# Kernel optimization log

Hardware: AMD Instinct MI355X
Metric: run time of the kernel (lower is better)

The kernel has to match this reference:

```python
import jax, jax.numpy as jnp
import numpy as np

B, S, D, H = 4, 1024, 2048, 16
DH = D // H  # 128
THETA = 10000.0


def setup_inputs() -> dict:
    key = jax.random.key(0)
    k1, k2, k3 = jax.random.split(key, 3)
    std_qkv = np.sqrt(2.0 / (D + 3 * D)).astype(np.float32)
    std_out = np.sqrt(2.0 / (D + D)).astype(np.float32)
    x = jax.random.normal(k1, (B, S, D), jnp.float32)
    w_qkv = jax.random.normal(k2, (D, 3 * D), jnp.float32) * std_qkv
    w_out = jax.random.normal(k3, (D, D), jnp.float32) * std_out
    # matrix-based RoPE table: [max_seq, d_head//2, 2, 2]
    freqs = jnp.arange(S, dtype=jnp.float32)[:, None] / THETA ** (
        2.0 * jnp.arange(DH // 2, dtype=jnp.float32) / DH)[None, :]
    eye = jnp.array([[1.0, 0.0], [0.0, 1.0]], jnp.float32)
    rot = jnp.array([[0.0, -1.0], [1.0, 0.0]], jnp.float32)
    rope_matrix = (jnp.cos(freqs)[:, :, None, None] * eye
                   + jnp.sin(freqs)[:, :, None, None] * rot)
    token_positions = jnp.arange(S, dtype=jnp.int32)
    return {"x": x, "w_qkv": w_qkv, "w_out": w_out,
            "rope_matrix": rope_matrix, "token_positions": token_positions}


def _apply_rope(t, pe):
    # t: [B, H, S, DH]; pe: [S, DH//2, 2, 2] (gathered by token_positions)
    tr = t.reshape(*t.shape[:-1], DH // 2, 2)  # interleaved (even, odd) pairs
    out = jnp.einsum('bhski,skoi->bhsko', tr, pe)
    return out.reshape(t.shape)


def reference(x, w_qkv, w_out, rope_matrix, token_positions):
    qkv = jnp.einsum('bsd,df->bsf', x, w_qkv)          # [B,S,3D]
    q, k, v = jnp.split(qkv, 3, axis=-1)
    to_heads = lambda t: t.reshape(B, S, H, DH).transpose(0, 2, 1, 3)
    q, k, v = to_heads(q), to_heads(k), to_heads(v)    # [B,H,S,DH]
    pe = rope_matrix[token_positions]                  # [S, DH//2, 2, 2]
    q = _apply_rope(q, pe)
    k = _apply_rope(k, pe)
    scores = jnp.einsum('bhqd,bhkd->bhqk', q, k) / np.float32(np.sqrt(DH))
    causal = jnp.tril(jnp.ones((S, S), dtype=bool))
    scores = jnp.where(causal, scores, -jnp.inf)
    attn = jax.nn.softmax(scores, axis=-1)
    ctx = jnp.einsum('bhqk,bhkd->bhqd', attn, v)       # [B,H,S,DH]
    ctx = ctx.transpose(0, 2, 1, 3).reshape(B, S, D)
    return jnp.einsum('bsd,df->bsf', ctx, w_out)
```

## Files before the change

### kernel.cpp

```cpp
#include <hip/hip_runtime.h>
#include <hip/hip_bf16.h>
#include <math.h>

#define Bn 4
#define Sn 1024
#define Dn 2048
#define Hn 16
#define DHn 128
#define BS (Bn * Sn)
#define QKVC (3 * Dn)

typedef __attribute__((ext_vector_type(8))) short short8;
typedef __attribute__((ext_vector_type(4))) float float4v;

__device__ inline unsigned short f2bf(float x) {
  union { float f; unsigned int u; } v; v.f = x;
  unsigned int r = v.u + 0x7fffu + ((v.u >> 16) & 1u);
  return (unsigned short)(r >> 16);
}
__device__ inline float bf2f(unsigned short b) {
  union { unsigned int u; float f; } v; v.u = ((unsigned int)b) << 16;
  return v.f;
}

__device__ __forceinline__ void gload16(const unsigned short* g, unsigned short* l) {
  __builtin_amdgcn_global_load_lds(
      (const __attribute__((address_space(1))) unsigned int*)g,
      (__attribute__((address_space(3))) unsigned int*)l, 16, 0, 0);
}

__global__ __launch_bounds__(256) void cvt_f32_bf16(
    const float* __restrict__ in, unsigned short* __restrict__ out, int n8) {
  int id = blockIdx.x * 256 + threadIdx.x;
  if (id >= n8) return;
  const float4* p = reinterpret_cast<const float4*>(in) + 2 * (size_t)id;
  float4 a = p[0], b = p[1];
  short8 o;
  o[0] = (short)f2bf(a.x); o[1] = (short)f2bf(a.y);
  o[2] = (short)f2bf(a.z); o[3] = (short)f2bf(a.w);
  o[4] = (short)f2bf(b.x); o[5] = (short)f2bf(b.y);
  o[6] = (short)f2bf(b.z); o[7] = (short)f2bf(b.w);
  *reinterpret_cast<short8*>(out + 8 * (size_t)id) = o;
}

__global__ __launch_bounds__(256) void transpose_cvt(
    const float* __restrict__ w, unsigned short* __restrict__ wT, int K, int N) {
  __shared__ unsigned short t[64][72];
  const int c0 = blockIdx.x * 64;
  const int r0 = blockIdx.y * 64;
  const int tid = threadIdx.x;
  const int r = tid >> 2;
  const int cb = (tid & 3) * 16;
#pragma unroll
  for (int it = 0; it < 4; ++it) {
    float4 v = *reinterpret_cast<const float4*>(&w[(long)(r0 + r) * N + c0 + cb + 4 * it]);
    t[r][cb + 4 * it + 0] = f2bf(v.x);
    t[r][cb + 4 * it + 1] = f2bf(v.y);
    t[r][cb + 4 * it + 2] = f2bf(v.z);
    t[r][cb + 4 * it + 3] = f2bf(v.w);
  }
  __syncthreads();
  unsigned short o[16];
#pragma unroll
  for (int e = 0; e < 16; ++e) o[e] = t[cb + e][r];
  unsigned short* dst = &wT[(long)(c0 + r) * K + r0 + cb];
  *reinterpret_cast<short8*>(dst) = *reinterpret_cast<short8*>(&o[0]);
  *reinterpret_cast<short8*>(dst + 8) = *reinterpret_cast<short8*>(&o[8]);
}

#define AB8(buf, h) ((buf) * 16384 + (h) * 8192)
#define BB8(buf) (32768 + (buf) * 8192)

#define VMW(n)                                                                 \
  asm volatile("s_waitcnt vmcnt(" #n ")" ::: "memory");                        \
  __builtin_amdgcn_sched_barrier(0);

#define PHASE(BUF, MIH, STAGE_STMT, WAIT_STMT)                                 \
  {                                                                            \
    __builtin_amdgcn_sched_barrier(0);                                         \
    short8 afr[2][2];                                                          \
    _Pragma("unroll") for (int mi2 = 0; mi2 < 2; ++mi2) {                      \
      const int mrow = wr * 64 + ((MIH) * 2 + mi2) * 16;                       \
      const int hh = mrow >> 7;                                                \
      const int rl = (mrow & 127) + c;                                         \
      _Pragma("unroll") for (int ks = 0; ks < 2; ++ks)                         \
        afr[mi2][ks] = *(const short8*)(lds + AB8(BUF, 0) + hh * 8192 +        \
            rl * 64 + (((ks * 4 + g) ^ cg7) << 3));                            \
    }                                                                          \
    if ((MIH) == 0) {                                                          \
      _Pragma("unroll") for (int ni = 0; ni < 4; ++ni)                         \
        _Pragma("unroll") for (int ks = 0; ks < 2; ++ks)                       \
          bfr[ni][ks] = *(const short8*)(lds + BB8(BUF) +                      \
              (wc * 64 + ni * 16 + c) * 64 + (((ks * 4 + g) ^ cg7) << 3));     \
    }                                                                          \
    STAGE_STMT;                                                                \
    __builtin_amdgcn_sched_barrier(0);                                         \
    __builtin_amdgcn_s_barrier();                                              \
    asm volatile("s_waitcnt lgkmcnt(0)" ::: "memory");                         \
    __builtin_amdgcn_sched_barrier(0);                                         \
    __builtin_amdgcn_s_setprio(1);                                             \
    _Pragma("unroll") for (int mi2 = 0; mi2 < 2; ++mi2)                        \
      _Pragma("unroll") for (int ni = 0; ni < 4; ++ni)                         \
        _Pragma("unroll") for (int ks = 0; ks < 2; ++ks)                       \
          acc[(MIH) * 2 + mi2][ni] = __builtin_amdgcn_mfma_f32_16x16x32_bf16(  \
              afr[mi2][ks], bfr[ni][ks], acc[(MIH) * 2 + mi2][ni], 0, 0, 0);   \
    __builtin_amdgcn_s_setprio(0);                                             \
    WAIT_STMT                                                                  \
    __builtin_amdgcn_s_barrier();                                              \
  }

#define GEMM_MAIN_LOOP(A_, BT_, K_)                                            \
  STAGE(A_ + (long)m0 * K_, AB8(0, 0));                                        \
  STAGE(A_ + (long)(m0 + 128) * K_, AB8(0, 1));                                \
  STAGE(BT_ + (long)n0 * K_, BB8(0));                                          \
  STAGE(BT_ + (long)n0 * K_ + 64, BB8(1));                                     \
  VMW(2)                                                                       \
  __builtin_amdgcn_s_barrier();                                                \
  for (int it2 = 0; it2 < nt / 2 - 1; ++it2) {                                 \
    const long T1 = (long)(2 * it2 + 1) * 64;                                  \
    const long T2 = (long)(2 * it2 + 2) * 64;                                  \
    const long T3 = (long)(2 * it2 + 3) * 64;                                  \
    PHASE(0, 0, STAGE(A_ + (long)m0 * K_ + T1, AB8(1, 0)), )                   \
    PHASE(0, 1,                                                                \
          { STAGE(A_ + (long)(m0 + 128) * K_ + T1, AB8(1, 1));                 \
            STAGE(BT_ + (long)n0 * K_ + T2, BB8(0)); }, VMW(2))                \
    PHASE(1, 0, STAGE(A_ + (long)m0 * K_ + T2, AB8(0, 0)), )                   \
    PHASE(1, 1,                                                                \
          { STAGE(A_ + (long)(m0 + 128) * K_ + T2, AB8(0, 1));                 \
            STAGE(BT_ + (long)n0 * K_ + T3, BB8(1)); }, VMW(2))                \
  }                                                                            \
  {                                                                            \
    const long TL = (long)(nt - 1) * 64;                                       \
    PHASE(0, 0, STAGE(A_ + (long)m0 * K_ + TL, AB8(1, 0)), )                   \
    PHASE(0, 1, STAGE(A_ + (long)(m0 + 128) * K_ + TL, AB8(1, 1)), VMW(0))     \
    PHASE(1, 0, {}, )                                                          \
    PHASE(1, 1, {}, )                                                          \
  }

__global__ __launch_bounds__(512, 2) void gemm_qkv(
    const unsigned short* __restrict__ A, const unsigned short* __restrict__ BT,
    const float* __restrict__ rope, const int* __restrict__ tpos,
    unsigned short* __restrict__ qR, unsigned short* __restrict__ kR,
    unsigned short* __restrict__ vT, int K) {
  __shared__ unsigned short lds[49152];
  const int tid = threadIdx.x;
  const int wid = tid >> 6, lane = tid & 63;
  const int c = lane & 15, g = lane >> 4;
  const int wr = wid >> 1, wc = wid & 1;
  const int cg7 = c & 7;

  const int nwg = gridDim.x * gridDim.y;
  const int bid = blockIdx.y * gridDim.x + blockIdx.x;
  const int swz = (bid & 7) * (nwg >> 3) + (bid >> 3);
  const int m0 = (swz % gridDim.x) * 256, n0 = (swz / gridDim.x) * 128;

  const int nt = K >> 6;

  float4v acc[4][4];
#pragma unroll
  for (int i = 0; i < 4; ++i)
#pragma unroll
    for (int j = 0; j < 4; ++j) acc[i][j] = (float4v){0.f, 0.f, 0.f, 0.f};
  short8 bfr[4][2];

  auto STAGE = [&](const unsigned short* gbase, int sbase) {
#pragma unroll
    for (int j = 0; j < 2; ++j) {
      const int ch = j * 512 + tid;
      const int r = ch >> 3;
      const int wo = (ch & 7) ^ (r & 7);
      gload16(gbase + (long)r * K + wo * 8, lds + sbase + j * 4096 + wid * 512);
    }
  };

  GEMM_MAIN_LOOP(A, BT, K)

  const int type = n0 >> 11;
  const int h = (n0 & 2047) >> 7;
  const long bh = (long)((m0 >> 10) * Hn + h);
  const int s0 = m0 & 1023;

  if (type == 2) {
#pragma unroll
    for (int mi = 0; mi < 4; ++mi)
#pragma unroll
      for (int ni = 0; ni < 4; ++ni)
#pragma unroll
        for (int j = 0; j < 4; ++j) {
          const int mm = wr * 64 + mi * 16 + g * 4 + j;
          const int nn = wc * 64 + ni * 16 + c;
          lds[nn * 264 + mm] = f2bf(acc[mi][ni][j]);
        }
    __syncthreads();
    unsigned short* dst = vT + bh * (long)DHn * Sn + s0;
#pragma unroll
    for (int it = 0; it < 8; ++it) {
      const int cid = it * 512 + tid;
      const int d = cid >> 5;
      const int sl = (cid & 31) * 8;
      short8 v = *reinterpret_cast<const short8*>(lds + d * 264 + sl);
      *reinterpret_cast<short8*>(dst + (long)d * Sn + sl) = v;
    }
  } else {
#pragma unroll
    for (int mi = 0; mi < 4; ++mi)
#pragma unroll
      for (int ni = 0; ni < 4; ++ni)
#pragma unroll
        for (int j = 0; j < 4; ++j) {
          const int mm = wr * 64 + mi * 16 + g * 4 + j;
          const int nn = wc * 64 + ni * 16 + c;
          lds[mm * 136 + nn] = f2bf(acc[mi][ni][j]);
        }
    __syncthreads();
    unsigned short* dst = (type == 0 ? qR : kR) + (bh * Sn + s0) * DHn;
    const float qsc = (type == 0) ? 0.1275174213f : 1.0f;
#pragma unroll
    for (int it = 0; it < 8; ++it) {
      const int cid = it * 512 + tid;
      const int r = cid >> 4;
      const int colc = (cid & 15) * 8;
      union { short8 v; unsigned short u[8]; } iw, ow;
      iw.v = *reinterpret_cast<const short8*>(lds + r * 136 + colc);
      const int pos = tpos[s0 + r];
      const float4* pe = reinterpret_cast<const float4*>(rope) +
                         (long)pos * 64 + (colc >> 1);
#pragma unroll
      for (int p = 0; p < 4; ++p) {
        const float4 m2 = pe[p];
        const float xx = bf2f(iw.u[2 * p]), yy = bf2f(iw.u[2 * p + 1]);
        ow.u[2 * p]     = f2bf((m2.x * xx + m2.y * yy) * qsc);
        ow.u[2 * p + 1] = f2bf((m2.z * xx + m2.w * yy) * qsc);
      }
      *reinterpret_cast<short8*>(dst + (long)r * DHn + colc) = ow.v;
    }
  }
}

__global__ __launch_bounds__(512, 2) void gemm_out(
    const unsigned short* __restrict__ A, const unsigned short* __restrict__ BT,
    float* __restrict__ Cout, int N, int K) {
  __shared__ unsigned short lds[49152];
  const int tid = threadIdx.x;
  const int wid = tid >> 6, lane = tid & 63;
  const int c = lane & 15, g = lane >> 4;
  const int wr = wid >> 1, wc = wid & 1;
  const int cg7 = c & 7;

  const int nwg = gridDim.x * gridDim.y;
  const int bid = blockIdx.y * gridDim.x + blockIdx.x;
  const int swz = (bid & 7) * (nwg >> 3) + (bid >> 3);
  const int m0 = (swz % gridDim.x) * 256, n0 = (swz / gridDim.x) * 128;

  const int nt = K >> 6;

  float4v acc[4][4];
#pragma unroll
  for (int i = 0; i < 4; ++i)
#pragma unroll
    for (int j = 0; j < 4; ++j) acc[i][j] = (float4v){0.f, 0.f, 0.f, 0.f};
  short8 bfr[4][2];

  auto STAGE = [&](const unsigned short* gbase, int sbase) {
#pragma unroll
    for (int j = 0; j < 2; ++j) {
      const int ch = j * 512 + tid;
      const int r = ch >> 3;
      const int wo = (ch & 7) ^ (r & 7);
      gload16(gbase + (long)r * K + wo * 8, lds + sbase + j * 4096 + wid * 512);
    }
  };

  GEMM_MAIN_LOOP(A, BT, K)

#pragma unroll
  for (int mi = 0; mi < 4; ++mi)
#pragma unroll
    for (int ni = 0; ni < 4; ++ni)
#pragma unroll
      for (int j = 0; j < 4; ++j) {
        const int m = m0 + wr * 64 + mi * 16 + g * 4 + j;
        const int n = n0 + wc * 64 + ni * 16 + c;
        Cout[(long)m * N + n] = acc[mi][ni][j];
      }
}
#undef PHASE
#undef GEMM_MAIN_LOOP

__global__ __launch_bounds__(256, 2) void attn_mfma(
    const unsigned short* __restrict__ qR, const unsigned short* __restrict__ kR,
    const unsigned short* __restrict__ vTd, unsigned short* __restrict__ ctx) {
  __shared__ unsigned short lds[32768];
  __shared__ unsigned short Ps[4][16][72];
  const int qp = gridDim.x - 1 - blockIdx.x;
  const int h = blockIdx.y, b = blockIdx.z;
  const int tid = threadIdx.x, wid = tid >> 6, lane = tid & 63;
  const int c = lane & 15, g = lane >> 4, cg7 = c & 7;
  const long bh = (long)(b * Hn + h);
  const unsigned short* kbase = kR + bh * Sn * DHn;
  const unsigned short* vbase = vTd + bh * DHn * Sn;

  short8 qf[2][4];
#pragma unroll
  for (int sub = 0; sub < 2; ++sub) {
    const unsigned short* qrow =
        qR + (bh * Sn + qp * 128 + sub * 64 + wid * 16 + c) * DHn;
#pragma unroll
    for (int kc = 0; kc < 4; ++kc)
      qf[sub][kc] = *reinterpret_cast<const short8*>(qrow + kc * 32 + g * 8);
  }

  auto STAGE = [&](int kt, int buf) {
#pragma unroll
    for (int j = 0; j < 4; ++j) {
      const int ch = j * 256 + tid;
      const int r = ch >> 4, wd = ch & 15;
      const int ws = (wd & 8) | ((wd & 7) ^ (r & 7));
      gload16(kbase + (long)kt * 8192 + r * 128 + ws * 8,
              lds + buf * 8192 + j * 2048 + wid * 512);
    }
#pragma unroll
    for (int j = 0; j < 4; ++j) {
      const int ch = j * 256 + tid;
      const int d = ch >> 3, sw = ch & 7;
      gload16(vbase + (long)d * Sn + kt * 64 + ((sw ^ (d & 7)) << 3),
              lds + 16384 + buf * 8192 + j * 2048 + wid * 512);
    }
  };

  float m[2] = {-INFINITY, -INFINITY}, lsum[2] = {0.f, 0.f};
  float4v otA[8], otB[8];
#pragma unroll
  for (int fd = 0; fd < 8; ++fd) {
    otA[fd] = (float4v){0.f, 0.f, 0.f, 0.f};
    otB[fd] = (float4v){0.f, 0.f, 0.f, 0.f};
  }

  const int ntt = 2 * qp + 2;
  STAGE(0, 0);
  __syncthreads();
  int cur = 0;

  for (int kt = 0; kt < ntt; ++kt) {
    if (kt + 1 < ntt) STAGE(kt + 1, cur ^ 1);

#pragma unroll
    for (int sub = 0; sub < 2; ++sub) {
      if (sub == 0 && kt == ntt - 1) continue;
      float4v* ot = (sub == 0) ? otA : otB;

      float4v scv[4];
#pragma unroll
      for (int f = 0; f < 4; ++f) scv[f] = (float4v){0.f, 0.f, 0.f, 0.f};
      __builtin_amdgcn_s_setprio(1);
#pragma unroll
      for (int f = 0; f < 4; ++f)
#pragma unroll
        for (int kc = 0; kc < 4; ++kc) {
          const int wp = kc * 4 + g;
          const int ws = (wp & 8) | ((wp & 7) ^ cg7);
          short8 kf = *reinterpret_cast<const short8*>(
              lds + cur * 8192 + (f * 16 + c) * 128 + ws * 8);
          scv[f] = __builtin_amdgcn_mfma_f32_16x16x32_bf16(kf, qf[sub][kc],
                                                           scv[f], 0, 0, 0);
        }
      __builtin_amdgcn_s_setprio(0);

      if (kt == 2 * qp + sub) {
        const int qloc = wid * 16 + c;
#pragma unroll
        for (int f = 0; f < 4; ++f)
#pragma unroll
          for (int j = 0; j < 4; ++j)
            if (f * 16 + g * 4 + j > qloc) scv[f][j] = -INFINITY;
      }

      float tmax = -INFINITY;
#pragma unroll
      for (int f = 0; f < 4; ++f)
#pragma unroll
        for (int j = 0; j < 4; ++j) tmax = fmaxf(tmax, scv[f][j]);
      tmax = fmaxf(tmax, __shfl_xor(tmax, 16));
      tmax = fmaxf(tmax, __shfl_xor(tmax, 32));

      float mnew, corr;
      if (__all(tmax <= m[sub] + 8.f)) {
        mnew = m[sub]; corr = 1.f;
      } else {
        mnew = fmaxf(m[sub], tmax);
        corr = exp2f(m[sub] - mnew);
#pragma unroll
        for (int fd = 0; fd < 8; ++fd) ot[fd] *= corr;
      }
      float psum = 0.f;
#pragma unroll
      for (int f = 0; f < 4; ++f)
#pragma unroll
        for (int j = 0; j < 4; ++j) {
          scv[f][j] = exp2f(scv[f][j] - mnew);
          psum += scv[f][j];
        }
      psum += __shfl_xor(psum, 16);
      psum += __shfl_xor(psum, 32);
      lsum[sub] = lsum[sub] * corr + psum;
      m[sub] = mnew;

#pragma unroll
      for (int f = 0; f < 4; ++f) {
        unsigned int lo = (unsigned)f2bf(scv[f][0]) | ((unsigned)f2bf(scv[f][1]) << 16);
        unsigned int hi = (unsigned)f2bf(scv[f][2]) | ((unsigned)f2bf(scv[f][3]) << 16);
        uint2 pk; pk.x = lo; pk.y = hi;
        *reinterpret_cast<uint2*>(&Ps[wid][c][f * 16 + g * 4]) = pk;
      }

      short8 pf0 = *reinterpret_cast<const short8*>(&Ps[wid][c][g * 8]);
      short8 pf1 = *reinterpret_cast<const short8*>(&Ps[wid][c][32 + g * 8]);
      __builtin_amdgcn_s_setprio(1);
#pragma unroll
      for (int fd = 0; fd < 8; ++fd) {
        short8 vf0 = *reinterpret_cast<const short8*>(
            lds + 16384 + cur * 8192 + (fd * 16 + c) * 64 + ((g ^ cg7) << 3));
        short8 vf1 = *reinterpret_cast<const short8*>(
            lds + 16384 + cur * 8192 + (fd * 16 + c) * 64 + (((g + 4) ^ cg7) << 3));
        ot[fd] = __builtin_amdgcn_mfma_f32_16x16x32_bf16(vf0, pf0, ot[fd], 0, 0, 0);
        ot[fd] = __builtin_amdgcn_mfma_f32_16x16x32_bf16(vf1, pf1, ot[fd], 0, 0, 0);
      }
      __builtin_amdgcn_s_setprio(0);
    }

    __syncthreads();
    cur ^= 1;
  }

#pragma unroll
  for (int sub = 0; sub < 2; ++sub) {
    const float4v* ot = (sub == 0) ? otA : otB;
    const float inv = 1.0f / lsum[sub];
    unsigned short* orow =
        ctx + (long)(b * Sn + qp * 128 + sub * 64 + wid * 16 + c) * Dn + h * DHn;
#pragma unroll
    for (int fd = 0; fd < 8; ++fd) {
      const int d = fd * 16 + g * 4;
      uint2 pk;
      pk.x = (unsigned)f2bf(ot[fd][0] * inv) | ((unsigned)f2bf(ot[fd][1] * inv) << 16);
      pk.y = (unsigned)f2bf(ot[fd][2] * inv) | ((unsigned)f2bf(ot[fd][3] * inv) << 16);
      *reinterpret_cast<uint2*>(orow + d) = pk;
    }
  }
}

extern "C" void kernel_launch(void* const* d_in, const int* in_sizes, int n_in,
                              void* d_out, int out_size, void* d_ws, size_t ws_size,
                              hipStream_t stream) {
  const float* x     = (const float*)d_in[0];
  const float* w_qkv = (const float*)d_in[1];
  const float* w_out = (const float*)d_in[2];
  const float* rope  = (const float*)d_in[3];
  const int*   tpos  = (const int*)d_in[4];
  float* out = (float*)d_out;

  unsigned short* x16    = (unsigned short*)d_ws;
  unsigned short* wqkvT  = x16 + (size_t)BS * Dn;
  unsigned short* woutT  = wqkvT + (size_t)Dn * QKVC;
  unsigned short* qR     = woutT + (size_t)Dn * Dn;
  unsigned short* kR     = qR + (size_t)BS * Dn;
  unsigned short* vT16   = kR + (size_t)BS * Dn;
  unsigned short* ctx16  = vT16 + (size_t)BS * Dn;

  cvt_f32_bf16<<<(BS * Dn / 8 + 255) / 256, 256, 0, stream>>>(x, x16, BS * Dn / 8);
  {
    dim3 g1(QKVC / 64, Dn / 64);
    transpose_cvt<<<g1, 256, 0, stream>>>(w_qkv, wqkvT, Dn, QKVC);
    dim3 g2(Dn / 64, Dn / 64);
    transpose_cvt<<<g2, 256, 0, stream>>>(w_out, woutT, Dn, Dn);
  }
  {
    dim3 grid(BS / 256, QKVC / 128);
    gemm_qkv<<<grid, 512, 0, stream>>>(x16, wqkvT, rope, tpos, qR, kR, vT16, Dn);
  }
  {
    dim3 grid(Sn / 128, Hn, Bn);
    attn_mfma<<<grid, 256, 0, stream>>>(qR, kR, vT16, ctx16);
  }
  {
    dim3 grid(BS / 256, Dn / 128);
    gemm_out<<<grid, 512, 0, stream>>>(ctx16, woutT, out, Dn, Dn);
  }
}
```

Baseline: 255.2 us.

## Switch GEMMs to 32x32x16 MFMA and merge preprocessing kernels into one launch

Result: no change. 257.4 us (+0.9%).

```diff
diff --git a/kernel.cpp b/kernel.cpp
--- a/kernel.cpp
+++ b/kernel.cpp
@@ -12,6 +12,7 @@
 
 typedef __attribute__((ext_vector_type(8))) short short8;
 typedef __attribute__((ext_vector_type(4))) float float4v;
+typedef __attribute__((ext_vector_type(16))) float float16v;
 
 __device__ inline unsigned short f2bf(float x) {
   union { float f; unsigned int u; } v; v.f = x;
@@ -29,26 +30,11 @@
       (__attribute__((address_space(3))) unsigned int*)l, 16, 0, 0);
 }
 
-__global__ __launch_bounds__(256) void cvt_f32_bf16(
-    const float* __restrict__ in, unsigned short* __restrict__ out, int n8) {
-  int id = blockIdx.x * 256 + threadIdx.x;
-  if (id >= n8) return;
-  const float4* p = reinterpret_cast<const float4*>(in) + 2 * (size_t)id;
-  float4 a = p[0], b = p[1];
-  short8 o;
-  o[0] = (short)f2bf(a.x); o[1] = (short)f2bf(a.y);
-  o[2] = (short)f2bf(a.z); o[3] = (short)f2bf(a.w);
-  o[4] = (short)f2bf(b.x); o[5] = (short)f2bf(b.y);
-  o[6] = (short)f2bf(b.z); o[7] = (short)f2bf(b.w);
-  *reinterpret_cast<short8*>(out + 8 * (size_t)id) = o;
-}
-
-__global__ __launch_bounds__(256) void transpose_cvt(
-    const float* __restrict__ w, unsigned short* __restrict__ wT, int K, int N) {
-  __shared__ unsigned short t[64][72];
-  const int c0 = blockIdx.x * 64;
-  const int r0 = blockIdx.y * 64;
-  const int tid = threadIdx.x;
+__device__ void tc_body(const float* __restrict__ w, unsigned short* __restrict__ wT,
+                        int K, int N, int bx, int by, int tid,
+                        unsigned short (*t)[72]) {
+  const int c0 = bx * 64;
+  const int r0 = by * 64;
   const int r = tid >> 2;
   const int cb = (tid & 3) * 16;
 #pragma unroll
@@ -68,6 +54,32 @@
   *reinterpret_cast<short8*>(dst + 8) = *reinterpret_cast<short8*>(&o[8]);
 }
 
+__global__ __launch_bounds__(256) void prep_all(
+    const float* __restrict__ x, const float* __restrict__ w_qkv,
+    const float* __restrict__ w_out, unsigned short* __restrict__ x16,
+    unsigned short* __restrict__ wqkvT, unsigned short* __restrict__ woutT) {
+  __shared__ unsigned short t[64][72];
+  const int bid = blockIdx.x;
+  const int tid = threadIdx.x;
+  if (bid < 4096) {
+    const int id = bid * 256 + tid;
+    const float4* p = reinterpret_cast<const float4*>(x) + 2 * (size_t)id;
+    float4 a = p[0], b = p[1];
+    short8 o;
+    o[0] = (short)f2bf(a.x); o[1] = (short)f2bf(a.y);
+    o[2] = (short)f2bf(a.z); o[3] = (short)f2bf(a.w);
+    o[4] = (short)f2bf(b.x); o[5] = (short)f2bf(b.y);
+    o[6] = (short)f2bf(b.z); o[7] = (short)f2bf(b.w);
+    *reinterpret_cast<short8*>(x16 + 8 * (size_t)id) = o;
+  } else if (bid < 7168) {
+    const int lb = bid - 4096;
+    tc_body(w_qkv, wqkvT, Dn, QKVC, lb % 96, lb / 96, tid, t);
+  } else {
+    const int lb = bid - 7168;
+    tc_body(w_out, woutT, Dn, Dn, lb % 32, lb / 32, tid, t);
+  }
+}
+
 #define AB8(buf, h) ((buf) * 16384 + (h) * 8192)
 #define BB8(buf) (32768 + (buf) * 8192)
 
@@ -75,35 +87,34 @@
   asm volatile("s_waitcnt vmcnt(" #n ")" ::: "memory");                        \
   __builtin_amdgcn_sched_barrier(0);
 
-#define PHASE(BUF, MIH, STAGE_STMT, WAIT_STMT)                                 \
+#define PHASE(BUF, KH, STAGE_STMT, WAIT_STMT)                                  \
   {                                                                            \
     __builtin_amdgcn_sched_barrier(0);                                         \
-    short8 afr[2][2];                                                          \
-    _Pragma("unroll") for (int mi2 = 0; mi2 < 2; ++mi2) {                      \
-      const int mrow = wr * 64 + ((MIH) * 2 + mi2) * 16;                       \
-      const int hh = mrow >> 7;                                                \
-      const int rl = (mrow & 127) + c;                                         \
-      _Pragma("unroll") for (int ks = 0; ks < 2; ++ks)                         \
-        afr[mi2][ks] = *(const short8*)(lds + AB8(BUF, 0) + hh * 8192 +        \
-            rl * 64 + (((ks * 4 + g) ^ cg7) << 3));                            \
-    }                                                                          \
-    if ((MIH) == 0) {                                                          \
-      _Pragma("unroll") for (int ni = 0; ni < 4; ++ni)                         \
-        _Pragma("unroll") for (int ks = 0; ks < 2; ++ks)                       \
-          bfr[ni][ks] = *(const short8*)(lds + BB8(BUF) +                      \
-              (wc * 64 + ni * 16 + c) * 64 + (((ks * 4 + g) ^ cg7) << 3));     \
-    }                                                                          \
+    short8 afr[2][2], bfr2[2][2];                                              \
+    _Pragma("unroll") for (int m2 = 0; m2 < 2; ++m2)                           \
+      _Pragma("unroll") for (int kk = 0; kk < 2; ++kk) {                       \
+        const int arow = wr * 64 + m2 * 32 + l31;                              \
+        const int hh = arow >> 7, rl = arow & 127;                             \
+        afr[m2][kk] = *(const short8*)(lds + AB8(BUF, 0) + hh * 8192 +         \
+            rl * 64 + ((((KH) * 4 + kk * 2 + hi) ^ w7) << 3));                 \
+      }                                                                        \
+    _Pragma("unroll") for (int n2 = 0; n2 < 2; ++n2)                           \
+      _Pragma("unroll") for (int kk = 0; kk < 2; ++kk) {                       \
+        const int brow = wc * 64 + n2 * 32 + l31;                              \
+        bfr2[n2][kk] = *(const short8*)(lds + BB8(BUF) + brow * 64 +           \
+            ((((KH) * 4 + kk * 2 + hi) ^ w7) << 3));                           \
+      }                                                                        \
     STAGE_STMT;                                                                \
     __builtin_amdgcn_sched_barrier(0);                                         \
     __builtin_amdgcn_s_barrier();                                              \
     asm volatile("s_waitcnt lgkmcnt(0)" ::: "memory");                         \
     __builtin_amdgcn_sched_barrier(0);                                         \
     __builtin_amdgcn_s_setprio(1);                                             \
-    _Pragma("unroll") for (int mi2 = 0; mi2 < 2; ++mi2)                        \
-      _Pragma("unroll") for (int ni = 0; ni < 4; ++ni)                         \
-        _Pragma("unroll") for (int ks = 0; ks < 2; ++ks)                       \
-          acc[(MIH) * 2 + mi2][ni] = __builtin_amdgcn_mfma_f32_16x16x32_bf16(  \
-              afr[mi2][ks], bfr[ni][ks], acc[(MIH) * 2 + mi2][ni], 0, 0, 0);   \
+    _Pragma("unroll") for (int kk = 0; kk < 2; ++kk)                           \
+      _Pragma("unroll") for (int m2 = 0; m2 < 2; ++m2)                         \
+        _Pragma("unroll") for (int n2 = 0; n2 < 2; ++n2)                       \
+          acc[m2][n2] = __builtin_amdgcn_mfma_f32_32x32x16_bf16(               \
+              afr[m2][kk], bfr2[n2][kk], acc[m2][n2], 0, 0, 0);                \
     __builtin_amdgcn_s_setprio(0);                                             \
     WAIT_STMT                                                                  \
     __builtin_amdgcn_s_barrier();                                              \
@@ -145,9 +156,8 @@
   __shared__ unsigned short lds[49152];
   const int tid = threadIdx.x;
   const int wid = tid >> 6, lane = tid & 63;
-  const int c = lane & 15, g = lane >> 4;
+  const int l31 = lane & 31, hi = lane >> 5, w7 = l31 & 7;
   const int wr = wid >> 1, wc = wid & 1;
-  const int cg7 = c & 7;
 
   const int nwg = gridDim.x * gridDim.y;
   const int bid = blockIdx.y * gridDim.x + blockIdx.x;
@@ -156,12 +166,13 @@
 
   const int nt = K >> 6;
 
-  float4v acc[4][4];
-#pragma unroll
-  for (int i = 0; i < 4; ++i)
-#pragma unroll
-    for (int j = 0; j < 4; ++j) acc[i][j] = (float4v){0.f, 0.f, 0.f, 0.f};
-  short8 bfr[4][2];
+  float16v acc[2][2];
+#pragma unroll
+  for (int i = 0; i < 2; ++i)
+#pragma unroll
+    for (int j = 0; j < 2; ++j)
+#pragma unroll
+      for (int r = 0; r < 16; ++r) acc[i][j][r] = 0.f;
 
   auto STAGE = [&](const unsigned short* gbase, int sbase) {
 #pragma unroll
@@ -182,14 +193,14 @@
 
   if (type == 2) {
 #pragma unroll
-    for (int mi = 0; mi < 4; ++mi)
-#pragma unroll
-      for (int ni = 0; ni < 4; ++ni)
-#pragma unroll
-        for (int j = 0; j < 4; ++j) {
-          const int mm = wr * 64 + mi * 16 + g * 4 + j;
-          const int nn = wc * 64 + ni * 16 + c;
-          lds[nn * 264 + mm] = f2bf(acc[mi][ni][j]);
+    for (int m2 = 0; m2 < 2; ++m2)
+#pragma unroll
+      for (int n2 = 0; n2 < 2; ++n2)
+#pragma unroll
+        for (int r = 0; r < 16; ++r) {
+          const int mm = wr * 64 + m2 * 32 + (r & 3) + 8 * (r >> 2) + 4 * hi;
+          const int nn = wc * 64 + n2 * 32 + l31;
+          lds[nn * 264 + mm] = f2bf(acc[m2][n2][r]);
         }
     __syncthreads();
     unsigned short* dst = vT + bh * (long)DHn * Sn + s0;
@@ -203,14 +214,14 @@
     }
   } else {
 #pragma unroll
-    for (int mi = 0; mi < 4; ++mi)
-#pragma unroll
-      for (int ni = 0; ni < 4; ++ni)
-#pragma unroll
-        for (int j = 0; j < 4; ++j) {
-          const int mm = wr * 64 + mi * 16 + g * 4 + j;
-          const int nn = wc * 64 + ni * 16 + c;
-          lds[mm * 136 + nn] = f2bf(acc[mi][ni][j]);
+    for (int m2 = 0; m2 < 2; ++m2)
+#pragma unroll
+      for (int n2 = 0; n2 < 2; ++n2)
+#pragma unroll
+        for (int r = 0; r < 16; ++r) {
+          const int mm = wr * 64 + m2 * 32 + (r & 3) + 8 * (r >> 2) + 4 * hi;
+          const int nn = wc * 64 + n2 * 32 + l31;
+          lds[mm * 136 + nn] = f2bf(acc[m2][n2][r]);
         }
     __syncthreads();
     unsigned short* dst = (type == 0 ? qR : kR) + (bh * Sn + s0) * DHn;
@@ -227,10 +238,10 @@
                          (long)pos * 64 + (colc >> 1);
 #pragma unroll
       for (int p = 0; p < 4; ++p) {
-        const float4 m2 = pe[p];
+        const float4 m2v = pe[p];
         const float xx = bf2f(iw.u[2 * p]), yy = bf2f(iw.u[2 * p + 1]);
-        ow.u[2 * p]     = f2bf((m2.x * xx + m2.y * yy) * qsc);
-        ow.u[2 * p + 1] = f2bf((m2.z * xx + m2.w * yy) * qsc);
+        ow.u[2 * p]     = f2bf((m2v.x * xx + m2v.y * yy) * qsc);
+        ow.u[2 * p + 1] = f2bf((m2v.z * xx + m2v.w * yy) * qsc);
       }
       *reinterpret_cast<short8*>(dst + (long)r * DHn + colc) = ow.v;
     }
@@ -243,9 +254,8 @@
   __shared__ unsigned short lds[49152];
   const int tid = threadIdx.x;
   const int wid = tid >> 6, lane = tid & 63;
-  const int c = lane & 15, g = lane >> 4;
+  const int l31 = lane & 31, hi = lane >> 5, w7 = l31 & 7;
   const int wr = wid >> 1, wc = wid & 1;
-  const int cg7 = c & 7;
 
   const int nwg = gridDim.x * gridDim.y;
   const int bid = blockIdx.y * gridDim.x + blockIdx.x;
@@ -254,12 +264,13 @@
 
   const int nt = K >> 6;
 
-  float4v acc[4][4];
-#pragma unroll
-  for (int i = 0; i < 4; ++i)
-#pragma unroll
-    for (int j = 0; j < 4; ++j) acc[i][j] = (float4v){0.f, 0.f, 0.f, 0.f};
-  short8 bfr[4][2];
+  float16v acc[2][2];
+#pragma unroll
+  for (int i = 0; i < 2; ++i)
+#pragma unroll
+    for (int j = 0; j < 2; ++j)
+#pragma unroll
+      for (int r = 0; r < 16; ++r) acc[i][j][r] = 0.f;
 
   auto STAGE = [&](const unsigned short* gbase, int sbase) {
 #pragma unroll
@@ -274,14 +285,14 @@
   GEMM_MAIN_LOOP(A, BT, K)
 
 #pragma unroll
-  for (int mi = 0; mi < 4; ++mi)
-#pragma unroll
-    for (int ni = 0; ni < 4; ++ni)
-#pragma unroll
-      for (int j = 0; j < 4; ++j) {
-        const int m = m0 + wr * 64 + mi * 16 + g * 4 + j;
-        const int n = n0 + wc * 64 + ni * 16 + c;
-        Cout[(long)m * N + n] = acc[mi][ni][j];
+  for (int m2 = 0; m2 < 2; ++m2)
+#pragma unroll
+    for (int n2 = 0; n2 < 2; ++n2)
+#pragma unroll
+      for (int r = 0; r < 16; ++r) {
+        const int mm = wr * 64 + m2 * 32 + (r & 3) + 8 * (r >> 2) + 4 * hi;
+        const int nn = wc * 64 + n2 * 32 + l31;
+        Cout[(long)(m0 + mm) * N + n0 + nn] = acc[m2][n2][r];
       }
 }
 #undef PHASE
@@ -408,8 +419,8 @@
 #pragma unroll
       for (int f = 0; f < 4; ++f) {
         unsigned int lo = (unsigned)f2bf(scv[f][0]) | ((unsigned)f2bf(scv[f][1]) << 16);
-        unsigned int hi = (unsigned)f2bf(scv[f][2]) | ((unsigned)f2bf(scv[f][3]) << 16);
-        uint2 pk; pk.x = lo; pk.y = hi;
+        unsigned int hi2 = (unsigned)f2bf(scv[f][2]) | ((unsigned)f2bf(scv[f][3]) << 16);
+        uint2 pk; pk.x = lo; pk.y = hi2;
         *reinterpret_cast<uint2*>(&Ps[wid][c][f * 16 + g * 4]) = pk;
       }
 
@@ -467,13 +478,7 @@
   unsigned short* vT16   = kR + (size_t)BS * Dn;
   unsigned short* ctx16  = vT16 + (size_t)BS * Dn;
 
-  cvt_f32_bf16<<<(BS * Dn / 8 + 255) / 256, 256, 0, stream>>>(x, x16, BS * Dn / 8);
-  {
-    dim3 g1(QKVC / 64, Dn / 64);
-    transpose_cvt<<<g1, 256, 0, stream>>>(w_qkv, wqkvT, Dn, QKVC);
-    dim3 g2(Dn / 64, Dn / 64);
-    transpose_cvt<<<g2, 256, 0, stream>>>(w_out, woutT, Dn, Dn);
-  }
+  prep_all<<<8192, 256, 0, stream>>>(x, w_qkv, w_out, x16, wqkvT, woutT);
   {
     dim3 grid(BS / 256, QKVC / 128);
     gemm_qkv<<<grid, 512, 0, stream>>>(x16, wqkvT, rope, tpos, qR, kR, vT16, Dn);
```
